# Optimization experiments

Hardware: AMD Instinct MI355X
Metric: run time of the kernel (lower is better)

The kernel has to match this reference:

```python
import jax, jax.numpy as jnp
import numpy as np

H = 768       # hidden_size
NH = 12       # num query heads
NKV = 4       # num kv heads
HD = 64       # head_dim
EPS = 1e-12

def setup_inputs() -> dict:
    key = jax.random.key(0)
    ks = jax.random.split(key, 6)
    s = 0.02
    return {
        "hidden_states": jax.random.normal(ks[0], (2, 2048, H), dtype=jnp.float32),
        "Wq": jax.random.normal(ks[1], (H, H), dtype=jnp.float32) * s,
        "bq": jnp.zeros((H,), jnp.float32),
        "Wk": jax.random.normal(ks[2], (H, NKV * HD), dtype=jnp.float32) * s,
        "bk": jnp.zeros((NKV * HD,), jnp.float32),
        "Wv": jax.random.normal(ks[3], (H, NKV * HD), dtype=jnp.float32) * s,
        "bv": jnp.zeros((NKV * HD,), jnp.float32),
        "Wo": jax.random.normal(ks[4], (H, H), dtype=jnp.float32) * s,
        "bo": jnp.zeros((H,), jnp.float32),
        "gamma": jnp.ones((H,), jnp.float32),
        "beta": jnpp if False else jnp.zeros((H,), jnp.float32),
    }

def _rope_tables(seq_len):
    # freqs over half the head dim, base 10000 (matches _init_rope)
    freqs = 1.0 / (10000.0 ** (jnp.arange(0, HD, 2, dtype=jnp.float32) / HD))  # [HD/2]
    t = jnp.arange(seq_len, dtype=jnp.float32)
    ang = jnp.outer(t, freqs)  # [S, HD/2]
    return jnp.cos(ang), jnp.sin(ang)

def _apply_rope(x, cos, sin):
    # x: [B, S, nheads, HD]; cos/sin: [S, HD/2] broadcast to [1, S, 1, HD/2]
    c = cos[None, :, None, :]
    s = sin[None, :, None, :]
    x1, x2 = x[..., : HD // 2], x[..., HD // 2 :]
    return jnp.concatenate([x1 * c - x2 * s, x1 * s + x2 * c], axis=-1)

def reference(hidden_states, Wq, bq, Wk, bk, Wv, bv, Wo, bo, gamma, beta):
    B, S, _ = hidden_states.shape
    residual = hidden_states
    # LayerNorm (eps=1e-12)
    mu = jnp.mean(hidden_states, axis=-1, keepdims=True)
    var = jnp.mean((hidden_states - mu) ** 2, axis=-1, keepdims=True)
    h = (hidden_states - mu) / jnp.sqrt(var + EPS) * gamma + beta
    q = (h @ Wq + bq).reshape(B, S, NH, HD)
    k = (h @ Wk + bk).reshape(B, S, NKV, HD)
    v = (h @ Wv + bv).reshape(B, S, NKV, HD)
    cos, sin = _rope_tables(S)
    q = _apply_rope(q, cos, sin)
    k = _apply_rope(k, cos, sin)
    # GQA: repeat_interleave kv heads to match query heads
    rep = NH // NKV
    k = jnp.repeat(k, rep, axis=2)  # [B,S,NH,HD]
    v = jnp.repeat(v, rep, axis=2)
    # [B,NH,S,S] scores
    scores = jnp.einsum("bqhd,bkhd->bhqk", q, k) / jnp.sqrt(jnp.float32(HD))
    attn = jax.nn.softmax(scores, axis=-1)
    out = jnp.einsum("bhqk,bkhd->bqhd", attn, v).reshape(B, S, H)
    out = out @ Wo + bo
    return residual + out
```

## Files before the change

kernel.cpp:

```cpp
#include <hip/hip_runtime.h>

typedef short bf16x8 __attribute__((ext_vector_type(8)));
typedef float f32x4 __attribute__((ext_vector_type(4)));
typedef float f32x16 __attribute__((ext_vector_type(16)));
typedef unsigned u32x4 __attribute__((ext_vector_type(4)));

#define SWZ(r, cb) ((((int)(r)) << 7) + (((int)(cb)) ^ ((((int)(r)) & 7) << 4)))

__device__ __forceinline__ unsigned short f2b(float f) {
    unsigned u = __builtin_bit_cast(unsigned, f);
    u = (u + 0x7FFFu + ((u >> 16) & 1u)) >> 16;
    return (unsigned short)u;
}
__device__ __forceinline__ float b2f(unsigned short h) {
    unsigned u = ((unsigned)h) << 16;
    return __builtin_bit_cast(float, u);
}
__device__ __forceinline__ void gload16(void* lds, const void* gsrc) {
    __builtin_amdgcn_global_load_lds((const __attribute__((address_space(1))) void*)gsrc,
                                     (__attribute__((address_space(3))) void*)lds, 16, 0, 0);
}

__global__ __launch_bounds__(256) void ln_kernel(const float* __restrict__ x,
                                                 const float* __restrict__ gamma,
// ... 60 lines not shown
        tile[kr][nc + 0] = f.x; tile[kr][nc + 1] = f.y;
        tile[kr][nc + 2] = f.z; tile[kr][nc + 3] = f.w;
    }
    __syncthreads();
#pragma unroll
    for (int i = 0; i < 2; i++) {
        int nr = (t >> 3) + i * 32, kc = (t & 7) * 8;
        bf16x8 o;
#pragma unroll
        for (int j = 0; j < 8; j++) o[j] = (short)f2b(tile[kc + j][nr]);
        *(bf16x8*)(WT + (size_t)(n0 + nr) * 768 + k0 + kc) = o;
    }
}

__global__ __launch_bounds__(256) void gemm_qkv(const unsigned short* __restrict__ A,
                                                const unsigned short* __restrict__ WqT,
                                                const unsigned short* __restrict__ WkT,
                                                const unsigned short* __restrict__ WvT,
                                                const float* __restrict__ bq,
                                                const float* __restrict__ bk,
                                                const float* __restrict__ bv,
                                                unsigned short* __restrict__ qo,
                                                unsigned short* __restrict__ kfrag,
                                                unsigned short* __restrict__ vfrag) {
    __shared__ __align__(1024) char smem[65536];
    const int m0 = blockIdx.x * 128;
    const int n0 = blockIdx.y * 128;
    const unsigned short* WT; const float* bias; int c0;
    if (n0 < 768)       { WT = WqT + (size_t)n0 * 768;          bias = bq; c0 = n0;        }
    else if (n0 < 1024) { WT = WkT + (size_t)(n0 - 768) * 768;  bias = bk; c0 = n0 - 768;  }
    else                { WT = WvT + (size_t)(n0 - 1024) * 768; bias = bv; c0 = n0 - 1024; }
    const int tid = threadIdx.x, lane = tid & 63, w = tid >> 6;
    const int wr = w >> 1, wc = w & 1;
    const int l15 = lane & 15;
    const int rl = lane >> 3, cl = lane & 7;
    const int scol = (cl * 16) ^ (rl << 4);

    const char* srcA0 = (const char*)A  + (size_t)(m0 + w * 32 +  0 + rl) * 1536 + scol;
    const char* srcA1 = (const char*)A  + (size_t)(m0 + w * 32 +  8 + rl) * 1536 + scol;
    const char* srcA2 = (const char*)A  + (size_t)(m0 + w * 32 + 16 + rl) * 1536 + scol;
    const char* srcA3 = (const char*)A  + (size_t)(m0 + w * 32 + 24 + rl) * 1536 + scol;
    const char* srcB0 = (const char*)WT + (size_t)(w * 32 +  0 + rl) * 1536 + scol;
    const char* srcB1 = (const char*)WT + (size_t)(w * 32 +  8 + rl) * 1536 + scol;
    const char* srcB2 = (const char*)WT + (size_t)(w * 32 + 16 + rl) * 1536 + scol;
    const char* srcB3 = (const char*)WT + (size_t)(w * 32 + 24 + rl) * 1536 + scol;
    const int cb = w * 4096;

    f32x4 acc[4][4];
#pragma unroll
    for (int m = 0; m < 4; m++)
#pragma unroll
        for (int n = 0; n < 4; n++) acc[m][n] = (f32x4){0.f, 0.f, 0.f, 0.f};

    gload16(smem + cb +    0, srcA0); gload16(smem + cb + 1024, srcA1);
    gload16(smem + cb + 2048, srcA2); gload16(smem + cb + 3072, srcA3);
    gload16(smem + 32768 + cb +    0, srcB0); gload16(smem + 32768 + cb + 1024, srcB1);
    gload16(smem + 32768 + cb + 2048, srcB2); gload16(smem + 32768 + cb + 3072, srcB3);
    __syncthreads();

    for (int t = 0; t < 12; ++t) {
        const int cur = t & 1;
        if (t < 11) {
            srcA0 += 128; srcA1 += 128; srcA2 += 128; srcA3 += 128;
            srcB0 += 128; srcB1 += 128; srcB2 += 128; srcB3 += 128;
            char* ab = smem + (cur ^ 1) * 16384 + cb;
            char* bb = smem + 32768 + (cur ^ 1) * 16384 + cb;
            gload16(ab +    0, srcA0); gload16(ab + 1024, srcA1);
            gload16(ab + 2048, srcA2); gload16(ab + 3072, srcA3);
            gload16(bb +    0, srcB0); gload16(bb + 1024, srcB1);
            gload16(bb + 2048, srcB2); gload16(bb + 3072, srcB3);
        }
        const char* Ab = smem + cur * 16384;
        const char* Bb = smem + 32768 + cur * 16384;
#pragma unroll
        for (int ks = 0; ks < 2; ks++) {
            bf16x8 a[4], b[4];
#pragma unroll
            for (int m = 0; m < 4; m++)
                a[m] = *(const bf16x8*)(Ab + SWZ(wr * 64 + m * 16 + l15, (lane >> 4) * 16 + ks * 64));
#pragma unroll
            for (int n = 0; n < 4; n++)
                b[n] = *(const bf16x8*)(Bb + SWZ(wc * 64 + n * 16 + l15, (lane >> 4) * 16 + ks * 64));
#pragma unroll
            for (int m = 0; m < 4; m++)
#pragma unroll
                for (int n = 0; n < 4; n++)
                    acc[m][n] = __builtin_amdgcn_mfma_f32_16x16x32_bf16(a[m], b[n], acc[m][n], 0, 0, 0);
        }
        __syncthreads();
    }

    if (n0 >= 1024) {
#pragma unroll
        for (int n = 0; n < 4; n++) {
            int col = c0 + wc * 64 + n * 16 + l15;
            float bs = bias[col];
            int g = col >> 6, d = col & 63;
            int hd = d >> 5, ld = d & 31;
#pragma unroll
            for (int m = 0; m < 4; m++) {
                int row = m0 + wr * 64 + m * 16 + ((lane >> 4) << 2);
                int bb2 = row >> 11, srow = row & 2047;
                int tt = srow >> 6, kvc = srow & 63;
                int s = kvc >> 4, hl = (kvc >> 3) & 1, j0 = kvc & 7;
                ushort4 o;
                o.x = f2b(acc[m][n][0] + bs); o.y = f2b(acc[m][n][1] + bs);
                o.z = f2b(acc[m][n][2] + bs); o.w = f2b(acc[m][n][3] + bs);
                *(ushort4*)((char*)vfrag + ((size_t)((bb2 * 4 + g) * 32 + tt)) * 8192 +
                            (2 * s + hd) * 1024 + (hl * 32 + ld) * 16 + j0 * 2) = o;
            }
        }
    } else if (n0 >= 768) {
#pragma unroll
        for (int n = 0; n < 2; n++) {
            int col = c0 + wc * 64 + n * 16 + l15;
            float bs1 = bias[col], bs2 = bias[col + 32];
            int g = col >> 6, i = col & 63;
            float freq = exp2f(-(float)i * (13.287712379549449f / 32.0f));
            int s = i >> 4, h2k = (i >> 3) & 1, j = i & 7;
            int laneoff = (h2k * 32 + 0) * 16 + j * 2;
#pragma unroll
            for (int m = 0; m < 4; m++) {
#pragma unroll
                for (int r = 0; r < 4; r++) {
                    int row = m0 + wr * 64 + m * 16 + ((lane >> 4) << 2) + r;
                    int bb2 = row >> 11, srow = row & 2047;
                    int tt = srow >> 6, kvr = srow & 63, hk = kvr >> 5, lkv = kvr & 31;
                    float sn, cs;
                    sincosf((float)srow * freq, &sn, &cs);
                    float x1 = acc[m][n][r] + bs1, x2 = acc[m][n + 2][r] + bs2;
                    size_t base = ((size_t)((bb2 * 4 + g) * 32 + tt)) * 8192 + laneoff + lkv * 16;
                    *(unsigned short*)((char*)kfrag + base + (2 * s + hk) * 1024)     = f2b(x1 * cs - x2 * sn);
                    *(unsigned short*)((char*)kfrag + base + (2 * s + 4 + hk) * 1024) = f2b(x1 * sn + x2 * cs);
                }
            }
        }
    } else {
#pragma unroll
        for (int n = 0; n < 4; n++) {
            int col = c0 + wc * 64 + n * 16 + l15;
            float bs = bias[col];
#pragma unroll
            for (int m = 0; m < 4; m++) {
#pragma unroll
                for (int r = 0; r < 4; r++) {
                    int row = m0 + wr * 64 + m * 16 + ((lane >> 4) << 2) + r;
                    qo[(size_t)row * 768 + col] = f2b(acc[m][n][r] + bs);
                }
            }
        }
    }
}

__global__ __launch_bounds__(768) void flashkv_kernel(const unsigned short* __restrict__ qb,
                                                      const unsigned short* __restrict__ kfrag,
                                                      const unsigned short* __restrict__ vfrag,
                                                      unsigned short* __restrict__ ob) {
    __shared__ __align__(1024) char smem[65536];
    const int s0 = blockIdx.x * 64;
    const int bg = blockIdx.y, b = bg >> 2;
    const int tid = threadIdx.x, lane = tid & 63, w = tid >> 6;
    const int h2 = lane >> 5, l31 = lane & 31;
    const int hq = w >> 2, qsub = (w >> 1) & 1, half = w & 1;
    const int hh = (bg & 3) * 3 + hq;

    const char* kf = (const char*)kfrag + (size_t)bg * 262144;
    const char* vf = (const char*)vfrag + (size_t)bg * 262144;
    const int ncha = (w < 8) ? 3 : 2;
    const char* srcs[3]; int ldss[3];
#pragma unroll
    for (int i = 0; i < 3; i++) {
        int c = w + i * 12;
        if (c < 32) {
            int hf = c >> 4, cc = c & 15;
            const char* basep = (cc < 8) ? kf : vf;
            srcs[i] = basep + (size_t)(hf * 16) * 8192 + (cc & 7) * 1024 + lane * 16;
            ldss[i] = hf * 32768 + ((cc < 8) ? 0 : 16384) + (cc & 7) * 1024;
        } else { srcs[i] = kf; ldss[i] = 0; }
    }

#pragma unroll
    for (int i = 0; i < 3; i++)
        if (i < ncha) gload16(smem + ldss[i], srcs[i]);

    const int qrow = s0 + qsub * 32 + l31;
    const unsigned short* qbase = qb + ((size_t)(b * 2048 + qrow) * 12 + hh) * 64 + 8 * h2;
    bf16x8 qr[4];
#pragma unroll
    for (int s = 0; s < 4; s++) qr[s] = *(const bf16x8*)(qbase + 16 * s);
    bf16x8 bqf[4];
    {
        const float SC = 0.125f * 1.4426950408889634f;
#pragma unroll
        for (int s = 0; s < 2; s++)
#pragma unroll
            for (int j = 0; j < 8; j++) {
                int i = 16 * s + 8 * h2 + j;
                float freq = exp2f(-(float)i * (13.287712379549449f / 32.0f));
                float sn, cs;
                sincosf((float)qrow * freq, &sn, &cs);
                float x1 = b2f((unsigned short)qr[s][j]);
                float x2 = b2f((unsigned short)qr[s + 2][j]);
                bqf[s][j]     = (short)f2b((x1 * cs - x2 * sn) * SC);
                bqf[s + 2][j] = (short)f2b((x1 * sn + x2 * cs) * SC);
            }
    }

    f32x16 accO0, accO1, cinit;
#pragma unroll
    for (int r = 0; r < 16; r++) { accO0[r] = 0.f; accO1[r] = 0.f; cinit[r] = -24.0f; }
    float l_r = 0.f;

    __syncthreads();

    for (int t = 0; t < 16; ++t) {
        const int cur = t & 1;
        if (t < 15) {
            const int nb = (cur ^ 1) * 8192;
#pragma unroll
            for (int i = 0; i < 3; i++)
                if (i < ncha) { srcs[i] += 8192; gload16(smem + ldss[i] + nb, srcs[i]); }
        }
        const char* kb_ = smem + half * 32768 + cur * 8192 + lane * 16;
        const char* vb_ = smem + half * 32768 + 16384 + cur * 8192 + lane * 16;

        f32x16 sc0, sc1;
        __builtin_amdgcn_s_setprio(1);
        sc0 = __builtin_amdgcn_mfma_f32_32x32x16_bf16(*(const bf16x8*)(kb_ + 0),    bqf[0], cinit, 0, 0, 0);
        sc1 = __builtin_amdgcn_mfma_f32_32x32x16_bf16(*(const bf16x8*)(kb_ + 1024), bqf[0], cinit, 0, 0, 0);
#pragma unroll
        for (int s = 1; s < 4; s++) {
            sc0 = __builtin_amdgcn_mfma_f32_32x32x16_bf16(*(const bf16x8*)(kb_ + s * 2048),        bqf[s], sc0, 0, 0, 0);
            sc1 = __builtin_amdgcn_mfma_f32_32x32x16_bf16(*(const bf16x8*)(kb_ + s * 2048 + 1024), bqf[s], sc1, 0, 0, 0);
        }
        __builtin_amdgcn_s_setprio(0);

#pragma unroll
        for (int r = 0; r < 16; r++) { sc0[r] = __builtin_amdgcn_exp2f(sc0[r]); }
#pragma unroll
        for (int r = 0; r < 16; r++) { sc1[r] = __builtin_amdgcn_exp2f(sc1[r]); }
        float ps[8];
#pragma unroll
        for (int r = 0; r < 8; r++)
            ps[r] = (sc0[r] + sc0[r + 8]) + (sc1[r] + sc1[r + 8]);
        float ls = ((ps[0] + ps[1]) + (ps[2] + ps[3])) + ((ps[4] + ps[5]) + (ps[6] + ps[7]));
        ls += __shfl_xor(ls, 32, 64);
        l_r += ls;

        __builtin_amdgcn_s_setprio(1);
#define DO_FRAG(SCX, OFF, S)                                                                  \
        {                                                                                     \
            unsigned A0, A1, B0, B1;                                                          \
            asm("v_cvt_pk_bf16_f32 %0, %1, %2" : "=v"(A0) : "v"(SCX[OFF + 0]), "v"(SCX[OFF + 1])); \
            asm("v_cvt_pk_bf16_f32 %0, %1, %2" : "=v"(A1) : "v"(SCX[OFF + 2]), "v"(SCX[OFF + 3])); \
            asm("v_cvt_pk_bf16_f32 %0, %1, %2" : "=v"(B0) : "v"(SCX[OFF + 4]), "v"(SCX[OFF + 5])); \
            asm("v_cvt_pk_bf16_f32 %0, %1, %2" : "=v"(B1) : "v"(SCX[OFF + 6]), "v"(SCX[OFF + 7])); \
            asm volatile("v_permlane32_swap_b32 %0, %1" : "+v"(A0), "+v"(B0));                 \
            asm volatile("v_permlane32_swap_b32 %0, %1" : "+v"(A1), "+v"(B1));                 \
            u32x4 fd = {A0, A1, B0, B1};                                                      \
            bf16x8 pa = __builtin_bit_cast(bf16x8, fd);                                       \
            bf16x8 bv0 = *(const bf16x8*)(vb_ + (S) * 2048);                                  \
            bf16x8 bv1 = *(const bf16x8*)(vb_ + (S) * 2048 + 1024);                           \
            accO0 = __builtin_amdgcn_mfma_f32_32x32x16_bf16(pa, bv0, accO0, 0, 0, 0);         \
            accO1 = __builtin_amdgcn_mfma_f32_32x32x16_bf16(pa, bv1, accO1, 0, 0, 0);         \
        }
        DO_FRAG(sc0, 0, 0)
        DO_FRAG(sc0, 8, 1)
        DO_FRAG(sc1, 0, 2)
        DO_FRAG(sc1, 8, 3)
#undef DO_FRAG
        __builtin_amdgcn_s_setprio(0);
        __syncthreads();
    }

    const int pr = w >> 1;
    if (half) {
        if (h2 == 0) *(float*)(smem + 49152 + pr * 128 + l31 * 4) = l_r;
#pragma unroll
        for (int pc = 0; pc < 4; pc++) {
            float4 f0;
            f0.x = accO0[4 * pc]; f0.y = accO0[4 * pc + 1];
            f0.z = accO0[4 * pc + 2]; f0.w = accO0[4 * pc + 3];
            *(float4*)(smem + pr * 8192 + pc * 1024 + lane * 16) = f0;
            float4 f1;
            f1.x = accO1[4 * pc]; f1.y = accO1[4 * pc + 1];
            f1.z = accO1[4 * pc + 2]; f1.w = accO1[4 * pc + 3];
            *(float4*)(smem + pr * 8192 + (4 + pc) * 1024 + lane * 16) = f1;
        }
    }
    __syncthreads();
    if (!half) {
        float lt = l_r + *(const float*)(smem + 49152 + pr * 128 + l31 * 4);
        f32x16 po0, po1;
#pragma unroll
        for (int pc = 0; pc < 4; pc++) {
            float4 f0 = *(const float4*)(smem + pr * 8192 + pc * 1024 + lane * 16);
            po0[4 * pc] = f0.x; po0[4 * pc + 1] = f0.y; po0[4 * pc + 2] = f0.z; po0[4 * pc + 3] = f0.w;
            float4 f1 = *(const float4*)(smem + pr * 8192 + (4 + pc) * 1024 + lane * 16);
            po1[4 * pc] = f1.x; po1[4 * pc + 1] = f1.y; po1[4 * pc + 2] = f1.z; po1[4 * pc + 3] = f1.w;
        }
#pragma unroll
        for (int r = 0; r < 16; r++) {
            int qc = (r & 3) + 8 * (r >> 2) + 4 * h2;
            float lvr = __builtin_amdgcn_rcpf(__shfl(lt, qc, 64));
            int row = s0 + qsub * 32 + qc;
            size_t basei = ((size_t)(b * 2048 + row) * 12 + hh) * 64;
            ob[basei + l31]      = f2b((accO0[r] + po0[r]) * lvr);
            ob[basei + 32 + l31] = f2b((accO1[r] + po1[r]) * lvr);
        }
    }
}

__global__ __launch_bounds__(256) void gemm_out(const unsigned short* __restrict__ A,
                                                const unsigned short* __restrict__ WoT,
                                                const float* __restrict__ bo,
                                                const float* __restrict__ resid,
                                                float* __restrict__ out) {
    __shared__ __align__(1024) char smem[65536];
    const int m0 = blockIdx.x * 128;
    const int n0 = blockIdx.y * 128;
    const int tid = threadIdx.x, lane = tid & 63, w = tid >> 6;
    const int wr = w >> 1, wc = w & 1;
    const int rl = lane >> 3, cl = lane & 7;
    const int scol = (cl * 16) ^ (rl << 4);

    const char* srcA0 = (const char*)A + (size_t)(m0 + w * 32 +  0 + rl) * 1536 + scol;
    const char* srcA1 = (const char*)A + (size_t)(m0 + w * 32 +  8 + rl) * 1536 + scol;
    const char* srcA2 = (const char*)A + (size_t)(m0 + w * 32 + 16 + rl) * 1536 + scol;
    const char* srcA3 = (const char*)A + (size_t)(m0 + w * 32 + 24 + rl) * 1536 + scol;
    const char* srcB0 = (const char*)WoT + (size_t)(n0 + w * 32 +  0 + rl) * 1536 + scol;
    const char* srcB1 = (const char*)WoT + (size_t)(n0 + w * 32 +  8 + rl) * 1536 + scol;
    const char* srcB2 = (const char*)WoT + (size_t)(n0 + w * 32 + 16 + rl) * 1536 + scol;
    const char* srcB3 = (const char*)WoT + (size_t)(n0 + w * 32 + 24 + rl) * 1536 + scol;
    const int cb = w * 4096;

    f32x4 acc[4][4];
#pragma unroll
    for (int m = 0; m < 4; m++)
#pragma unroll
        for (int n = 0; n < 4; n++) acc[m][n] = (f32x4){0.f, 0.f, 0.f, 0.f};

    gload16(smem + cb +    0, srcA0); gload16(smem + cb + 1024, srcA1);
    gload16(smem + cb + 2048, srcA2); gload16(smem + cb + 3072, srcA3);
    gload16(smem + 32768 + cb +    0, srcB0); gload16(smem + 32768 + cb + 1024, srcB1);
    gload16(smem + 32768 + cb + 2048, srcB2); gload16(smem + 32768 + cb + 3072, srcB3);
    __syncthreads();

    for (int t = 0; t < 12; ++t) {
        const int cur = t & 1;
        if (t < 11) {
            srcA0 += 128; srcA1 += 128; srcA2 += 128; srcA3 += 128;
            srcB0 += 128; srcB1 += 128; srcB2 += 128; srcB3 += 128;
            char* ab = smem + (cur ^ 1) * 16384 + cb;
            char* bb = smem + 32768 + (cur ^ 1) * 16384 + cb;
            gload16(ab +    0, srcA0); gload16(ab + 1024, srcA1);
            gload16(ab + 2048, srcA2); gload16(ab + 3072, srcA3);
            gload16(bb +    0, srcB0); gload16(bb + 1024, srcB1);
            gload16(bb + 2048, srcB2); gload16(bb + 3072, srcB3);
        }
        const char* Ab = smem + cur * 16384;
        const char* Bb = smem + 32768 + cur * 16384;
#pragma unroll
        for (int ks = 0; ks < 2; ks++) {
            bf16x8 a[4], b[4];
#pragma unroll
            for (int m = 0; m < 4; m++)
                a[m] = *(const bf16x8*)(Ab + SWZ(wr * 64 + m * 16 + (lane & 15), (lane >> 4) * 16 + ks * 64));
#pragma unroll
            for (int n = 0; n < 4; n++)
                b[n] = *(const bf16x8*)(Bb + SWZ(wc * 64 + n * 16 + (lane & 15), (lane >> 4) * 16 + ks * 64));
#pragma unroll
            for (int m = 0; m < 4; m++)
#pragma unroll
                for (int n = 0; n < 4; n++)
                    acc[m][n] = __builtin_amdgcn_mfma_f32_16x16x32_bf16(a[m], b[n], acc[m][n], 0, 0, 0);
        }
        __syncthreads();
    }
#pragma unroll
    for (int n = 0; n < 4; n++) {
        int col = n0 + wc * 64 + n * 16 + (lane & 15);
        float bs = bo[col];
#pragma unroll
        for (int m = 0; m < 4; m++) {
#pragma unroll
            for (int r = 0; r < 4; r++) {
                int row = m0 + wr * 64 + m * 16 + ((lane >> 4) << 2) + r;
                out[(size_t)row * 768 + col] = acc[m][n][r] + bs + resid[(size_t)row * 768 + col];
            }
        }
    }
}

extern "C" void kernel_launch(void* const* d_in, const int* in_sizes, int n_in,
                              void* d_out, int out_size, void* d_ws, size_t ws_size,
                              hipStream_t stream) {
    const float* hs    = (const float*)d_in[0];
    const float* Wq    = (const float*)d_in[1];
    const float* bq    = (const float*)d_in[2];
    const float* Wk    = (const float*)d_in[3];
    const float* bk    = (const float*)d_in[4];
    const float* Wv    = (const float*)d_in[5];
    const float* bv    = (const float*)d_in[6];
    const float* Wo    = (const float*)d_in[7];
    const float* bo    = (const float*)d_in[8];
    const float* gamma = (const float*)d_in[9];
    const float* beta  = (const float*)d_in[10];
    float* out = (float*)d_out;

    char* p = (char*)d_ws;
    unsigned short* hbuf  = (unsigned short*)p; p += (size_t)4096 * 768 * 2;
    unsigned short* qbuf  = (unsigned short*)p; p += (size_t)4096 * 768 * 2;
    unsigned short* kfbuf = (unsigned short*)p; p += (size_t)4096 * 256 * 2;
    unsigned short* vfbuf = (unsigned short*)p; p += (size_t)4096 * 256 * 2;
    unsigned short* WqT = (unsigned short*)p; p += (size_t)768 * 768 * 2;
    unsigned short* WkT = (unsigned short*)p; p += (size_t)256 * 768 * 2;
    unsigned short* WvT = (unsigned short*)p; p += (size_t)256 * 768 * 2;
    unsigned short* WoT = (unsigned short*)p; p += (size_t)768 * 768 * 2;
    unsigned short* obuf = hbuf;

    ln_kernel<<<1024, 256, 0, stream>>>(hs, gamma, beta, hbuf);
    transw_kernel<<<dim3(12, 12, 4), 256, 0, stream>>>(Wq, Wk, Wv, Wo, WqT, WkT, WvT, WoT);
    gemm_qkv<<<dim3(32, 10), 256, 0, stream>>>(hbuf, WqT, WkT, WvT, bq, bk, bv, qbuf, kfbuf, vfbuf);
    flashkv_kernel<<<dim3(32, 8), 768, 0, stream>>>(qbuf, kfbuf, vfbuf, obuf);
    gemm_out<<<dim3(32, 6), 256, 0, stream>>>(obuf, WoT, bo, hs, out);
}
```

Measured before the change: 86.60 us.

## Process all three GQA query heads per wave to reuse each K/V fragment

The attention kernel drops from 768 threads (12 waves, one query head per wave) to 256 threads (4 waves), each wave handling all three query heads that share a KV head. Each K and V fragment read from LDS now feeds three MFMAs instead of one, which cuts LDS read traffic and reuses the RoPE sin/cos values across heads. The cost is far more registers per wave (six output accumulators plus three score tiles), fewer waves to hide latency, and each wave issuing eight async copies per tile instead of two or three.

Measured after the change: 94.06 us. 8.6% more time.

```diff
diff --git a/kernel.cpp b/kernel.cpp
--- a/kernel.cpp
+++ b/kernel.cpp
@@ -236,161 +236,217 @@
     }
 }
 
-__global__ __launch_bounds__(768) void flashkv_kernel(const unsigned short* __restrict__ qb,
-                                                      const unsigned short* __restrict__ kfrag,
-                                                      const unsigned short* __restrict__ vfrag,
-                                                      unsigned short* __restrict__ ob) {
+__global__ __launch_bounds__(256, 1) void flash4_kernel(const unsigned short* __restrict__ qb,
+                                                        const unsigned short* __restrict__ kfrag,
+                                                        const unsigned short* __restrict__ vfrag,
+                                                        unsigned short* __restrict__ ob) {
     __shared__ __align__(1024) char smem[65536];
     const int s0 = blockIdx.x * 64;
     const int bg = blockIdx.y, b = bg >> 2;
     const int tid = threadIdx.x, lane = tid & 63, w = tid >> 6;
     const int h2 = lane >> 5, l31 = lane & 31;
-    const int hq = w >> 2, qsub = (w >> 1) & 1, half = w & 1;
-    const int hh = (bg & 3) * 3 + hq;
+    const int qsub = w >> 1, half = w & 1;
+    const int hbase = (bg & 3) * 3;
 
     const char* kf = (const char*)kfrag + (size_t)bg * 262144;
     const char* vf = (const char*)vfrag + (size_t)bg * 262144;
-    const int ncha = (w < 8) ? 3 : 2;
-    const char* srcs[3]; int ldss[3];
-#pragma unroll
-    for (int i = 0; i < 3; i++) {
-        int c = w + i * 12;
-        if (c < 32) {
-            int hf = c >> 4, cc = c & 15;
-            const char* basep = (cc < 8) ? kf : vf;
-            srcs[i] = basep + (size_t)(hf * 16) * 8192 + (cc & 7) * 1024 + lane * 16;
-            ldss[i] = hf * 32768 + ((cc < 8) ? 0 : 16384) + (cc & 7) * 1024;
-        } else { srcs[i] = kf; ldss[i] = 0; }
-    }
-
-#pragma unroll
-    for (int i = 0; i < 3; i++)
-        if (i < ncha) gload16(smem + ldss[i], srcs[i]);
+    const char* srcs[8]; int ldss[8];
+#pragma unroll
+    for (int i = 0; i < 8; i++) {
+        int c = w + i * 4;
+        int hf = c >> 4, cc = c & 15;
+        const char* basep = (cc < 8) ? kf : vf;
+        srcs[i] = basep + (size_t)(hf * 16) * 8192 + (cc & 7) * 1024 + lane * 16;
+        ldss[i] = hf * 32768 + ((cc < 8) ? 0 : 16384) + (cc & 7) * 1024;
+    }
+#pragma unroll
+    for (int i = 0; i < 8; i++) gload16(smem + ldss[i], srcs[i]);
 
     const int qrow = s0 + qsub * 32 + l31;
-    const unsigned short* qbase = qb + ((size_t)(b * 2048 + qrow) * 12 + hh) * 64 + 8 * h2;
-    bf16x8 qr[4];
-#pragma unroll
-    for (int s = 0; s < 4; s++) qr[s] = *(const bf16x8*)(qbase + 16 * s);
-    bf16x8 bqf[4];
+    bf16x8 qf[3][4];
     {
         const float SC = 0.125f * 1.4426950408889634f;
+        float cs_[16], sn_[16];
 #pragma unroll
         for (int s = 0; s < 2; s++)
 #pragma unroll
             for (int j = 0; j < 8; j++) {
                 int i = 16 * s + 8 * h2 + j;
                 float freq = exp2f(-(float)i * (13.287712379549449f / 32.0f));
-                float sn, cs;
-                sincosf((float)qrow * freq, &sn, &cs);
-                float x1 = b2f((unsigned short)qr[s][j]);
-                float x2 = b2f((unsigned short)qr[s + 2][j]);
-                bqf[s][j]     = (short)f2b((x1 * cs - x2 * sn) * SC);
-                bqf[s + 2][j] = (short)f2b((x1 * sn + x2 * cs) * SC);
-            }
-    }
-
-    f32x16 accO0, accO1, cinit;
-#pragma unroll
-    for (int r = 0; r < 16; r++) { accO0[r] = 0.f; accO1[r] = 0.f; cinit[r] = -24.0f; }
-    float l_r = 0.f;
+                sincosf((float)qrow * freq, &sn_[s * 8 + j], &cs_[s * 8 + j]);
+            }
+#pragma unroll
+        for (int u = 0; u < 3; u++) {
+            const unsigned short* qbase = qb + ((size_t)(b * 2048 + qrow) * 12 + hbase + u) * 64 + 8 * h2;
+            bf16x8 q0 = *(const bf16x8*)(qbase);
+            bf16x8 q1 = *(const bf16x8*)(qbase + 16);
+            bf16x8 q2 = *(const bf16x8*)(qbase + 32);
+            bf16x8 q3 = *(const bf16x8*)(qbase + 48);
+#pragma unroll
+            for (int j = 0; j < 8; j++) {
+                float x1 = b2f((unsigned short)q0[j]), x2 = b2f((unsigned short)q2[j]);
+                qf[u][0][j] = (short)f2b((x1 * cs_[j] - x2 * sn_[j]) * SC);
+                qf[u][2][j] = (short)f2b((x1 * sn_[j] + x2 * cs_[j]) * SC);
+                float y1 = b2f((unsigned short)q1[j]), y2 = b2f((unsigned short)q3[j]);
+                qf[u][1][j] = (short)f2b((y1 * cs_[8 + j] - y2 * sn_[8 + j]) * SC);
+                qf[u][3][j] = (short)f2b((y1 * sn_[8 + j] + y2 * cs_[8 + j]) * SC);
+            }
+        }
+    }
+
+    f32x16 acc[3][2], cinit;
+#pragma unroll
+    for (int u = 0; u < 3; u++)
+#pragma unroll
+        for (int k = 0; k < 2; k++)
+#pragma unroll
+            for (int r = 0; r < 16; r++) acc[u][k][r] = 0.f;
+#pragma unroll
+    for (int r = 0; r < 16; r++) cinit[r] = -24.0f;
+    float lr0 = 0.f, lr1 = 0.f, lr2 = 0.f;
 
     __syncthreads();
+
+#define SUM16(V) (((((V)[0]+(V)[1])+((V)[2]+(V)[3]))+(((V)[4]+(V)[5])+((V)[6]+(V)[7]))) + \
+                  ((((V)[8]+(V)[9])+((V)[10]+(V)[11]))+(((V)[12]+(V)[13])+((V)[14]+(V)[15]))))
 
     for (int t = 0; t < 16; ++t) {
         const int cur = t & 1;
         if (t < 15) {
             const int nb = (cur ^ 1) * 8192;
 #pragma unroll
-            for (int i = 0; i < 3; i++)
-                if (i < ncha) { srcs[i] += 8192; gload16(smem + ldss[i] + nb, srcs[i]); }
+            for (int i = 0; i < 8; i++) { srcs[i] += 8192; gload16(smem + ldss[i] + nb, srcs[i]); }
         }
         const char* kb_ = smem + half * 32768 + cur * 8192 + lane * 16;
-        const char* vb_ = smem + half * 32768 + 16384 + cur * 8192 + lane * 16;
-
-        f32x16 sc0, sc1;
-        __builtin_amdgcn_s_setprio(1);
-        sc0 = __builtin_amdgcn_mfma_f32_32x32x16_bf16(*(const bf16x8*)(kb_ + 0),    bqf[0], cinit, 0, 0, 0);
-        sc1 = __builtin_amdgcn_mfma_f32_32x32x16_bf16(*(const bf16x8*)(kb_ + 1024), bqf[0], cinit, 0, 0, 0);
-#pragma unroll
-        for (int s = 1; s < 4; s++) {
-            sc0 = __builtin_amdgcn_mfma_f32_32x32x16_bf16(*(const bf16x8*)(kb_ + s * 2048),        bqf[s], sc0, 0, 0, 0);
-            sc1 = __builtin_amdgcn_mfma_f32_32x32x16_bf16(*(const bf16x8*)(kb_ + s * 2048 + 1024), bqf[s], sc1, 0, 0, 0);
-        }
-        __builtin_amdgcn_s_setprio(0);
-
-#pragma unroll
-        for (int r = 0; r < 16; r++) { sc0[r] = __builtin_amdgcn_exp2f(sc0[r]); }
-#pragma unroll
-        for (int r = 0; r < 16; r++) { sc1[r] = __builtin_amdgcn_exp2f(sc1[r]); }
-        float ps[8];
-#pragma unroll
-        for (int r = 0; r < 8; r++)
-            ps[r] = (sc0[r] + sc0[r + 8]) + (sc1[r] + sc1[r + 8]);
-        float ls = ((ps[0] + ps[1]) + (ps[2] + ps[3])) + ((ps[4] + ps[5]) + (ps[6] + ps[7]));
-        ls += __shfl_xor(ls, 32, 64);
-        l_r += ls;
-
-        __builtin_amdgcn_s_setprio(1);
-#define DO_FRAG(SCX, OFF, S)                                                                  \
-        {                                                                                     \
-            unsigned A0, A1, B0, B1;                                                          \
-            asm("v_cvt_pk_bf16_f32 %0, %1, %2" : "=v"(A0) : "v"(SCX[OFF + 0]), "v"(SCX[OFF + 1])); \
-            asm("v_cvt_pk_bf16_f32 %0, %1, %2" : "=v"(A1) : "v"(SCX[OFF + 2]), "v"(SCX[OFF + 3])); \
-            asm("v_cvt_pk_bf16_f32 %0, %1, %2" : "=v"(B0) : "v"(SCX[OFF + 4]), "v"(SCX[OFF + 5])); \
-            asm("v_cvt_pk_bf16_f32 %0, %1, %2" : "=v"(B1) : "v"(SCX[OFF + 6]), "v"(SCX[OFF + 7])); \
-            asm volatile("v_permlane32_swap_b32 %0, %1" : "+v"(A0), "+v"(B0));                 \
-            asm volatile("v_permlane32_swap_b32 %0, %1" : "+v"(A1), "+v"(B1));                 \
-            u32x4 fd = {A0, A1, B0, B1};                                                      \
-            bf16x8 pa = __builtin_bit_cast(bf16x8, fd);                                       \
-            bf16x8 bv0 = *(const bf16x8*)(vb_ + (S) * 2048);                                  \
-            bf16x8 bv1 = *(const bf16x8*)(vb_ + (S) * 2048 + 1024);                           \
-            accO0 = __builtin_amdgcn_mfma_f32_32x32x16_bf16(pa, bv0, accO0, 0, 0, 0);         \
-            accO1 = __builtin_amdgcn_mfma_f32_32x32x16_bf16(pa, bv1, accO1, 0, 0, 0);         \
-        }
-        DO_FRAG(sc0, 0, 0)
-        DO_FRAG(sc0, 8, 1)
-        DO_FRAG(sc1, 0, 2)
-        DO_FRAG(sc1, 8, 3)
-#undef DO_FRAG
-        __builtin_amdgcn_s_setprio(0);
+        const char* vb_ = kb_ + 16384;
+
+#pragma unroll
+        for (int kvb = 0; kvb < 2; kvb++) {
+            f32x16 s0c, s1c, s2c;
+            __builtin_amdgcn_s_setprio(1);
+            {
+                bf16x8 ak = *(const bf16x8*)(kb_ + kvb * 1024);
+                s0c = __builtin_amdgcn_mfma_f32_32x32x16_bf16(ak, qf[0][0], cinit, 0, 0, 0);
+                s1c = __builtin_amdgcn_mfma_f32_32x32x16_bf16(ak, qf[1][0], cinit, 0, 0, 0);
+                s2c = __builtin_amdgcn_mfma_f32_32x32x16_bf16(ak, qf[2][0], cinit, 0, 0, 0);
+            }
+#pragma unroll
+            for (int s = 1; s < 4; s++) {
+                bf16x8 ak = *(const bf16x8*)(kb_ + s * 2048 + kvb * 1024);
+                s0c = __builtin_amdgcn_mfma_f32_32x32x16_bf16(ak, qf[0][s], s0c, 0, 0, 0);
+                s1c = __builtin_amdgcn_mfma_f32_32x32x16_bf16(ak, qf[1][s], s1c, 0, 0, 0);
+                s2c = __builtin_amdgcn_mfma_f32_32x32x16_bf16(ak, qf[2][s], s2c, 0, 0, 0);
+            }
+            __builtin_amdgcn_s_setprio(0);
+
+#pragma unroll
+            for (int r = 0; r < 16; r++) s0c[r] = __builtin_amdgcn_exp2f(s0c[r]);
+#pragma unroll
+            for (int r = 0; r < 16; r++) s1c[r] = __builtin_amdgcn_exp2f(s1c[r]);
+#pragma unroll
+            for (int r = 0; r < 16; r++) s2c[r] = __builtin_amdgcn_exp2f(s2c[r]);
+            lr0 += SUM16(s0c); lr1 += SUM16(s1c); lr2 += SUM16(s2c);
+
+            __builtin_amdgcn_s_setprio(1);
+#pragma unroll
+            for (int sh = 0; sh < 2; sh++) {
+                const int off = sh * 8;
+                bf16x8 pa0, pa1, pa2;
+                {
+                    unsigned A0, A1, B0, B1;
+                    asm("v_cvt_pk_bf16_f32 %0, %1, %2" : "=v"(A0) : "v"(s0c[off + 0]), "v"(s0c[off + 1]));
+                    asm("v_cvt_pk_bf16_f32 %0, %1, %2" : "=v"(A1) : "v"(s0c[off + 2]), "v"(s0c[off + 3]));
+                    asm("v_cvt_pk_bf16_f32 %0, %1, %2" : "=v"(B0) : "v"(s0c[off + 4]), "v"(s0c[off + 5]));
+                    asm("v_cvt_pk_bf16_f32 %0, %1, %2" : "=v"(B1) : "v"(s0c[off + 6]), "v"(s0c[off + 7]));
+                    asm volatile("v_permlane32_swap_b32 %0, %1" : "+v"(A0), "+v"(B0));
+                    asm volatile("v_permlane32_swap_b32 %0, %1" : "+v"(A1), "+v"(B1));
+                    u32x4 fd = {A0, A1, B0, B1};
+                    pa0 = __builtin_bit_cast(bf16x8, fd);
+                }
+                {
+                    unsigned A0, A1, B0, B1;
+                    asm("v_cvt_pk_bf16_f32 %0, %1, %2" : "=v"(A0) : "v"(s1c[off + 0]), "v"(s1c[off + 1]));
+                    asm("v_cvt_pk_bf16_f32 %0, %1, %2" : "=v"(A1) : "v"(s1c[off + 2]), "v"(s1c[off + 3]));
+                    asm("v_cvt_pk_bf16_f32 %0, %1, %2" : "=v"(B0) : "v"(s1c[off + 4]), "v"(s1c[off + 5]));
+                    asm("v_cvt_pk_bf16_f32 %0, %1, %2" : "=v"(B1) : "v"(s1c[off + 6]), "v"(s1c[off + 7]));
+                    asm volatile("v_permlane32_swap_b32 %0, %1" : "+v"(A0), "+v"(B0));
+                    asm volatile("v_permlane32_swap_b32 %0, %1" : "+v"(A1), "+v"(B1));
+                    u32x4 fd = {A0, A1, B0, B1};
+                    pa1 = __builtin_bit_cast(bf16x8, fd);
+                }
+                {
+                    unsigned A0, A1, B0, B1;
+                    asm("v_cvt_pk_bf16_f32 %0, %1, %2" : "=v"(A0) : "v"(s2c[off + 0]), "v"(s2c[off + 1]));
+                    asm("v_cvt_pk_bf16_f32 %0, %1, %2" : "=v"(A1) : "v"(s2c[off + 2]), "v"(s2c[off + 3]));
+                    asm("v_cvt_pk_bf16_f32 %0, %1, %2" : "=v"(B0) : "v"(s2c[off + 4]), "v"(s2c[off + 5]));
+                    asm("v_cvt_pk_bf16_f32 %0, %1, %2" : "=v"(B1) : "v"(s2c[off + 6]), "v"(s2c[off + 7]));
+                    asm volatile("v_permlane32_swap_b32 %0, %1" : "+v"(A0), "+v"(B0));
+                    asm volatile("v_permlane32_swap_b32 %0, %1" : "+v"(A1), "+v"(B1));
+                    u32x4 fd = {A0, A1, B0, B1};
+                    pa2 = __builtin_bit_cast(bf16x8, fd);
+                }
+                bf16x8 bv0 = *(const bf16x8*)(vb_ + (kvb * 2 + sh) * 2048);
+                bf16x8 bv1 = *(const bf16x8*)(vb_ + (kvb * 2 + sh) * 2048 + 1024);
+                acc[0][0] = __builtin_amdgcn_mfma_f32_32x32x16_bf16(pa0, bv0, acc[0][0], 0, 0, 0);
+                acc[0][1] = __builtin_amdgcn_mfma_f32_32x32x16_bf16(pa0, bv1, acc[0][1], 0, 0, 0);
+                acc[1][0] = __builtin_amdgcn_mfma_f32_32x32x16_bf16(pa1, bv0, acc[1][0], 0, 0, 0);
+                acc[1][1] = __builtin_amdgcn_mfma_f32_32x32x16_bf16(pa1, bv1, acc[1][1], 0, 0, 0);
+                acc[2][0] = __builtin_amdgcn_mfma_f32_32x32x16_bf16(pa2, bv0, acc[2][0], 0, 0, 0);
+                acc[2][1] = __builtin_amdgcn_mfma_f32_32x32x16_bf16(pa2, bv1, acc[2][1], 0, 0, 0);
+            }
+            __builtin_amdgcn_s_setprio(0);
+        }
         __syncthreads();
     }
-
-    const int pr = w >> 1;
+#undef SUM16
+
+    lr0 += __shfl_xor(lr0, 32, 64);
+    lr1 += __shfl_xor(lr1, 32, 64);
+    lr2 += __shfl_xor(lr2, 32, 64);
+
     if (half) {
-        if (h2 == 0) *(float*)(smem + 49152 + pr * 128 + l31 * 4) = l_r;
-#pragma unroll
-        for (int pc = 0; pc < 4; pc++) {
-            float4 f0;
-            f0.x = accO0[4 * pc]; f0.y = accO0[4 * pc + 1];
-            f0.z = accO0[4 * pc + 2]; f0.w = accO0[4 * pc + 3];
-            *(float4*)(smem + pr * 8192 + pc * 1024 + lane * 16) = f0;
-            float4 f1;
-            f1.x = accO1[4 * pc]; f1.y = accO1[4 * pc + 1];
-            f1.z = accO1[4 * pc + 2]; f1.w = accO1[4 * pc + 3];
-            *(float4*)(smem + pr * 8192 + (4 + pc) * 1024 + lane * 16) = f1;
-        }
+        if (h2 == 0) {
+            *(float*)(smem + 49152 + (qsub * 3 + 0) * 128 + l31 * 4) = lr0;
+            *(float*)(smem + 49152 + (qsub * 3 + 1) * 128 + l31 * 4) = lr1;
+            *(float*)(smem + 49152 + (qsub * 3 + 2) * 128 + l31 * 4) = lr2;
+        }
+#pragma unroll
+        for (int u = 0; u < 3; u++)
+#pragma unroll
+            for (int k = 0; k < 2; k++)
+#pragma unroll
+                for (int pc = 0; pc < 4; pc++) {
+                    float4 f;
+                    f.x = acc[u][k][4 * pc + 0]; f.y = acc[u][k][4 * pc + 1];
+                    f.z = acc[u][k][4 * pc + 2]; f.w = acc[u][k][4 * pc + 3];
+                    *(float4*)(smem + qsub * 24576 + (u * 2 + k) * 4096 + pc * 1024 + lane * 16) = f;
+                }
     }
     __syncthreads();
     if (!half) {
-        float lt = l_r + *(const float*)(smem + 49152 + pr * 128 + l31 * 4);
-        f32x16 po0, po1;
-#pragma unroll
-        for (int pc = 0; pc < 4; pc++) {
-            float4 f0 = *(const float4*)(smem + pr * 8192 + pc * 1024 + lane * 16);
-            po0[4 * pc] = f0.x; po0[4 * pc + 1] = f0.y; po0[4 * pc + 2] = f0.z; po0[4 * pc + 3] = f0.w;
-            float4 f1 = *(const float4*)(smem + pr * 8192 + (4 + pc) * 1024 + lane * 16);
-            po1[4 * pc] = f1.x; po1[4 * pc + 1] = f1.y; po1[4 * pc + 2] = f1.z; po1[4 * pc + 3] = f1.w;
-        }
-#pragma unroll
-        for (int r = 0; r < 16; r++) {
-            int qc = (r & 3) + 8 * (r >> 2) + 4 * h2;
-            float lvr = __builtin_amdgcn_rcpf(__shfl(lt, qc, 64));
-            int row = s0 + qsub * 32 + qc;
-            size_t basei = ((size_t)(b * 2048 + row) * 12 + hh) * 64;
-            ob[basei + l31]      = f2b((accO0[r] + po0[r]) * lvr);
-            ob[basei + 32 + l31] = f2b((accO1[r] + po1[r]) * lvr);
+        float lt0 = lr0 + *(const float*)(smem + 49152 + (qsub * 3 + 0) * 128 + l31 * 4);
+        float lt1 = lr1 + *(const float*)(smem + 49152 + (qsub * 3 + 1) * 128 + l31 * 4);
+        float lt2 = lr2 + *(const float*)(smem + 49152 + (qsub * 3 + 2) * 128 + l31 * 4);
+#pragma unroll
+        for (int u = 0; u < 3; u++) {
+            f32x16 po0, po1;
+#pragma unroll
+            for (int pc = 0; pc < 4; pc++) {
+                float4 f0 = *(const float4*)(smem + qsub * 24576 + (u * 2 + 0) * 4096 + pc * 1024 + lane * 16);
+                po0[4 * pc + 0] = f0.x; po0[4 * pc + 1] = f0.y; po0[4 * pc + 2] = f0.z; po0[4 * pc + 3] = f0.w;
+                float4 f1 = *(const float4*)(smem + qsub * 24576 + (u * 2 + 1) * 4096 + pc * 1024 + lane * 16);
+                po1[4 * pc + 0] = f1.x; po1[4 * pc + 1] = f1.y; po1[4 * pc + 2] = f1.z; po1[4 * pc + 3] = f1.w;
+            }
+            float ltu = (u == 0) ? lt0 : ((u == 1) ? lt1 : lt2);
+#pragma unroll
+            for (int r = 0; r < 16; r++) {
+                int qc = (r & 3) + 8 * (r >> 2) + 4 * h2;
+                float lv = __builtin_amdgcn_rcpf(__shfl(ltu, qc, 64));
+                int row = s0 + qsub * 32 + qc;
+                size_t basei = ((size_t)(b * 2048 + row) * 12 + hbase + u) * 64;
+                ob[basei + l31]      = f2b((acc[u][0][r] + po0[r]) * lv);
+                ob[basei + 32 + l31] = f2b((acc[u][1][r] + po1[r]) * lv);
+            }
         }
     }
 }
@@ -506,6 +562,6 @@
     ln_kernel<<<1024, 256, 0, stream>>>(hs, gamma, beta, hbuf);
     transw_kernel<<<dim3(12, 12, 4), 256, 0, stream>>>(Wq, Wk, Wv, Wo, WqT, WkT, WvT, WoT);
     gemm_qkv<<<dim3(32, 10), 256, 0, stream>>>(hbuf, WqT, WkT, WvT, bq, bk, bv, qbuf, kfbuf, vfbuf);
-    flashkv_kernel<<<dim3(32, 8), 768, 0, stream>>>(qbuf, kfbuf, vfbuf, obuf);
+    flash4_kernel<<<dim3(32, 8), 256, 0, stream>>>(qbuf, kfbuf, vfbuf, obuf);
     gemm_out<<<dim3(32, 6), 256, 0, stream>>>(obuf, WoT, bo, hs, out);
 }
```

## Split attention KV range across four waves per head with 32-row query tiles

Applied to the files above, without the earlier changes.

The attention kernel now gives each block 32 query rows instead of 64, doubling the grid from 256 to 512 blocks. Each wave handles one head over a quarter of the key sequence, where before two waves split it in halves. The partial outputs and row sums are combined in a two-stage shared-memory reduction. The goal is better CU occupancy (512 blocks on a 256-CU part) and fewer scores per wave per iteration, at the cost of reloading K/V for twice as many blocks and extra reduction syncs.

After: 132.0 us. +52.4%, slower.

```diff
diff --git a/kernel.cpp b/kernel.cpp
--- a/kernel.cpp
+++ b/kernel.cpp
@@ -236,161 +236,185 @@
     }
 }
 
-__global__ __launch_bounds__(768) void flashkv_kernel(const unsigned short* __restrict__ qb,
-                                                      const unsigned short* __restrict__ kfrag,
-                                                      const unsigned short* __restrict__ vfrag,
-                                                      unsigned short* __restrict__ ob) {
+__global__ __launch_bounds__(768, 6) void flashq_kernel(const unsigned short* __restrict__ qb,
+                                                        const unsigned short* __restrict__ kfrag,
+                                                        const unsigned short* __restrict__ vfrag,
+                                                        unsigned short* __restrict__ ob) {
     __shared__ __align__(1024) char smem[65536];
-    const int s0 = blockIdx.x * 64;
+    const int s0 = blockIdx.x * 32;
     const int bg = blockIdx.y, b = bg >> 2;
     const int tid = threadIdx.x, lane = tid & 63, w = tid >> 6;
     const int h2 = lane >> 5, l31 = lane & 31;
-    const int hq = w >> 2, qsub = (w >> 1) & 1, half = w & 1;
+    const int hq = w >> 2, qt = w & 3;
     const int hh = (bg & 3) * 3 + hq;
 
-    const char* kf = (const char*)kfrag + (size_t)bg * 262144;
-    const char* vf = (const char*)vfrag + (size_t)bg * 262144;
-    const int ncha = (w < 8) ? 3 : 2;
-    const char* srcs[3]; int ldss[3];
-#pragma unroll
-    for (int i = 0; i < 3; i++) {
-        int c = w + i * 12;
-        if (c < 32) {
-            int hf = c >> 4, cc = c & 15;
-            const char* basep = (cc < 8) ? kf : vf;
-            srcs[i] = basep + (size_t)(hf * 16) * 8192 + (cc & 7) * 1024 + lane * 16;
-            ldss[i] = hf * 32768 + ((cc < 8) ? 0 : 16384) + (cc & 7) * 1024;
-        } else { srcs[i] = kf; ldss[i] = 0; }
-    }
-
-#pragma unroll
-    for (int i = 0; i < 3; i++)
-        if (i < ncha) gload16(smem + ldss[i], srcs[i]);
-
-    const int qrow = s0 + qsub * 32 + l31;
-    const unsigned short* qbase = qb + ((size_t)(b * 2048 + qrow) * 12 + hh) * 64 + 8 * h2;
-    bf16x8 qr[4];
-#pragma unroll
-    for (int s = 0; s < 4; s++) qr[s] = *(const bf16x8*)(qbase + 16 * s);
-    bf16x8 bqf[4];
+    const bool stager = (w < 8);
+    const int sj = w >> 1, isV = w & 1;
+    const char* gsrc0 = (isV ? (const char*)vfrag : (const char*)kfrag) + (size_t)bg * 262144 + lane * 16;
+    const long gstr  = isV ? 1024 : 2048;
+    const int  goff1 = isV ? 4096 : 1024;
+    const int  lds_st = sj * 16384 + (isV ? 4096 : 0);
+
+    if (stager) {
+        int T = sj * 16;
+        const char* gb = gsrc0 + (size_t)(T >> 1) * 8192 + (T & 1) * goff1;
+#pragma unroll
+        for (int i = 0; i < 4; i++) gload16(smem + lds_st + i * 1024, gb + i * gstr);
+    }
+
+    const int qrow = s0 + l31;
+    bf16x8 qf[4];
     {
         const float SC = 0.125f * 1.4426950408889634f;
-#pragma unroll
-        for (int s = 0; s < 2; s++)
-#pragma unroll
-            for (int j = 0; j < 8; j++) {
-                int i = 16 * s + 8 * h2 + j;
-                float freq = exp2f(-(float)i * (13.287712379549449f / 32.0f));
-                float sn, cs;
-                sincosf((float)qrow * freq, &sn, &cs);
-                float x1 = b2f((unsigned short)qr[s][j]);
-                float x2 = b2f((unsigned short)qr[s + 2][j]);
-                bqf[s][j]     = (short)f2b((x1 * cs - x2 * sn) * SC);
-                bqf[s + 2][j] = (short)f2b((x1 * sn + x2 * cs) * SC);
-            }
-    }
-
-    f32x16 accO0, accO1, cinit;
-#pragma unroll
-    for (int r = 0; r < 16; r++) { accO0[r] = 0.f; accO1[r] = 0.f; cinit[r] = -24.0f; }
-    float l_r = 0.f;
-
-    __syncthreads();
+        const unsigned short* qbase = qb + ((size_t)(b * 2048 + qrow) * 12 + hh) * 64 + 8 * h2;
+        bf16x8 q0 = *(const bf16x8*)(qbase);
+        bf16x8 q1 = *(const bf16x8*)(qbase + 16);
+        bf16x8 q2 = *(const bf16x8*)(qbase + 32);
+        bf16x8 q3 = *(const bf16x8*)(qbase + 48);
+#pragma unroll
+        for (int j = 0; j < 8; j++) {
+            int i0 = 8 * h2 + j;
+            float f0 = exp2f(-(float)i0 * (13.287712379549449f / 32.0f));
+            float sn0, cs0;
+            sincosf((float)qrow * f0, &sn0, &cs0);
+            float x1 = b2f((unsigned short)q0[j]), x2 = b2f((unsigned short)q2[j]);
+            qf[0][j] = (short)f2b((x1 * cs0 - x2 * sn0) * SC);
+            qf[2][j] = (short)f2b((x1 * sn0 + x2 * cs0) * SC);
+            int i1 = 16 + 8 * h2 + j;
+            float f1 = exp2f(-(float)i1 * (13.287712379549449f / 32.0f));
+            float sn1, cs1;
+            sincosf((float)qrow * f1, &sn1, &cs1);
+            float y1 = b2f((unsigned short)q1[j]), y2 = b2f((unsigned short)q3[j]);
+            qf[1][j] = (short)f2b((y1 * cs1 - y2 * sn1) * SC);
+            qf[3][j] = (short)f2b((y1 * sn1 + y2 * cs1) * SC);
+        }
+    }
+
+    f32x16 acc0, acc1, cinit;
+#pragma unroll
+    for (int r = 0; r < 16; r++) { acc0[r] = 0.f; acc1[r] = 0.f; cinit[r] = -24.0f; }
+    float lr = 0.f;
+
+    __syncthreads();
+
+#define SUM16(V) (((((V)[0]+(V)[1])+((V)[2]+(V)[3]))+(((V)[4]+(V)[5])+((V)[6]+(V)[7]))) + \
+                  ((((V)[8]+(V)[9])+((V)[10]+(V)[11]))+(((V)[12]+(V)[13])+((V)[14]+(V)[15]))))
 
     for (int t = 0; t < 16; ++t) {
         const int cur = t & 1;
-        if (t < 15) {
-            const int nb = (cur ^ 1) * 8192;
-#pragma unroll
-            for (int i = 0; i < 3; i++)
-                if (i < ncha) { srcs[i] += 8192; gload16(smem + ldss[i] + nb, srcs[i]); }
-        }
-        const char* kb_ = smem + half * 32768 + cur * 8192 + lane * 16;
-        const char* vb_ = smem + half * 32768 + 16384 + cur * 8192 + lane * 16;
-
-        f32x16 sc0, sc1;
+        if (t < 15 && stager) {
+            int T = sj * 16 + t + 1;
+            const char* gb = gsrc0 + (size_t)(T >> 1) * 8192 + (T & 1) * goff1;
+            char* ld = smem + lds_st + (cur ^ 1) * 8192;
+#pragma unroll
+            for (int i = 0; i < 4; i++) gload16(ld + i * 1024, gb + i * gstr);
+        }
+        const char* kb_ = smem + qt * 16384 + cur * 8192 + lane * 16;
+        const char* vb_ = kb_ + 4096;
+
+        f32x16 sc;
         __builtin_amdgcn_s_setprio(1);
-        sc0 = __builtin_amdgcn_mfma_f32_32x32x16_bf16(*(const bf16x8*)(kb_ + 0),    bqf[0], cinit, 0, 0, 0);
-        sc1 = __builtin_amdgcn_mfma_f32_32x32x16_bf16(*(const bf16x8*)(kb_ + 1024), bqf[0], cinit, 0, 0, 0);
-#pragma unroll
-        for (int s = 1; s < 4; s++) {
-            sc0 = __builtin_amdgcn_mfma_f32_32x32x16_bf16(*(const bf16x8*)(kb_ + s * 2048),        bqf[s], sc0, 0, 0, 0);
-            sc1 = __builtin_amdgcn_mfma_f32_32x32x16_bf16(*(const bf16x8*)(kb_ + s * 2048 + 1024), bqf[s], sc1, 0, 0, 0);
-        }
+        sc = __builtin_amdgcn_mfma_f32_32x32x16_bf16(*(const bf16x8*)(kb_), qf[0], cinit, 0, 0, 0);
+#pragma unroll
+        for (int s = 1; s < 4; s++)
+            sc = __builtin_amdgcn_mfma_f32_32x32x16_bf16(*(const bf16x8*)(kb_ + s * 1024), qf[s], sc, 0, 0, 0);
         __builtin_amdgcn_s_setprio(0);
 
 #pragma unroll
-        for (int r = 0; r < 16; r++) { sc0[r] = __builtin_amdgcn_exp2f(sc0[r]); }
-#pragma unroll
-        for (int r = 0; r < 16; r++) { sc1[r] = __builtin_amdgcn_exp2f(sc1[r]); }
-        float ps[8];
-#pragma unroll
-        for (int r = 0; r < 8; r++)
-            ps[r] = (sc0[r] + sc0[r + 8]) + (sc1[r] + sc1[r + 8]);
-        float ls = ((ps[0] + ps[1]) + (ps[2] + ps[3])) + ((ps[4] + ps[5]) + (ps[6] + ps[7]));
-        ls += __shfl_xor(ls, 32, 64);
-        l_r += ls;
+        for (int r = 0; r < 16; r++) sc[r] = __builtin_amdgcn_exp2f(sc[r]);
+        lr += SUM16(sc);
 
         __builtin_amdgcn_s_setprio(1);
-#define DO_FRAG(SCX, OFF, S)                                                                  \
-        {                                                                                     \
-            unsigned A0, A1, B0, B1;                                                          \
-            asm("v_cvt_pk_bf16_f32 %0, %1, %2" : "=v"(A0) : "v"(SCX[OFF + 0]), "v"(SCX[OFF + 1])); \
-            asm("v_cvt_pk_bf16_f32 %0, %1, %2" : "=v"(A1) : "v"(SCX[OFF + 2]), "v"(SCX[OFF + 3])); \
-            asm("v_cvt_pk_bf16_f32 %0, %1, %2" : "=v"(B0) : "v"(SCX[OFF + 4]), "v"(SCX[OFF + 5])); \
-            asm("v_cvt_pk_bf16_f32 %0, %1, %2" : "=v"(B1) : "v"(SCX[OFF + 6]), "v"(SCX[OFF + 7])); \
-            asm volatile("v_permlane32_swap_b32 %0, %1" : "+v"(A0), "+v"(B0));                 \
-            asm volatile("v_permlane32_swap_b32 %0, %1" : "+v"(A1), "+v"(B1));                 \
-            u32x4 fd = {A0, A1, B0, B1};                                                      \
-            bf16x8 pa = __builtin_bit_cast(bf16x8, fd);                                       \
-            bf16x8 bv0 = *(const bf16x8*)(vb_ + (S) * 2048);                                  \
-            bf16x8 bv1 = *(const bf16x8*)(vb_ + (S) * 2048 + 1024);                           \
-            accO0 = __builtin_amdgcn_mfma_f32_32x32x16_bf16(pa, bv0, accO0, 0, 0, 0);         \
-            accO1 = __builtin_amdgcn_mfma_f32_32x32x16_bf16(pa, bv1, accO1, 0, 0, 0);         \
-        }
-        DO_FRAG(sc0, 0, 0)
-        DO_FRAG(sc0, 8, 1)
-        DO_FRAG(sc1, 0, 2)
-        DO_FRAG(sc1, 8, 3)
-#undef DO_FRAG
+#pragma unroll
+        for (int sh = 0; sh < 2; sh++) {
+            const int off = sh * 8;
+            unsigned A0, A1, B0, B1;
+            asm("v_cvt_pk_bf16_f32 %0, %1, %2" : "=v"(A0) : "v"(sc[off + 0]), "v"(sc[off + 1]));
+            asm("v_cvt_pk_bf16_f32 %0, %1, %2" : "=v"(A1) : "v"(sc[off + 2]), "v"(sc[off + 3]));
+            asm("v_cvt_pk_bf16_f32 %0, %1, %2" : "=v"(B0) : "v"(sc[off + 4]), "v"(sc[off + 5]));
+            asm("v_cvt_pk_bf16_f32 %0, %1, %2" : "=v"(B1) : "v"(sc[off + 6]), "v"(sc[off + 7]));
+            asm volatile("v_permlane32_swap_b32 %0, %1" : "+v"(A0), "+v"(B0));
+            asm volatile("v_permlane32_swap_b32 %0, %1" : "+v"(A1), "+v"(B1));
+            u32x4 fd = {A0, A1, B0, B1};
+            bf16x8 pa = __builtin_bit_cast(bf16x8, fd);
+            bf16x8 bv0 = *(const bf16x8*)(vb_ + (2 * sh + 0) * 1024);
+            bf16x8 bv1 = *(const bf16x8*)(vb_ + (2 * sh + 1) * 1024);
+            acc0 = __builtin_amdgcn_mfma_f32_32x32x16_bf16(pa, bv0, acc0, 0, 0, 0);
+            acc1 = __builtin_amdgcn_mfma_f32_32x32x16_bf16(pa, bv1, acc1, 0, 0, 0);
+        }
         __builtin_amdgcn_s_setprio(0);
         __syncthreads();
     }
-
-    const int pr = w >> 1;
-    if (half) {
-        if (h2 == 0) *(float*)(smem + 49152 + pr * 128 + l31 * 4) = l_r;
+#undef SUM16
+
+    lr += __shfl_xor(lr, 32, 64);
+
+    if (qt >= 2) {
+        int slot = hq * 2 + (qt - 2);
 #pragma unroll
         for (int pc = 0; pc < 4; pc++) {
             float4 f0;
-            f0.x = accO0[4 * pc]; f0.y = accO0[4 * pc + 1];
-            f0.z = accO0[4 * pc + 2]; f0.w = accO0[4 * pc + 3];
-            *(float4*)(smem + pr * 8192 + pc * 1024 + lane * 16) = f0;
+            f0.x = acc0[4 * pc + 0]; f0.y = acc0[4 * pc + 1];
+            f0.z = acc0[4 * pc + 2]; f0.w = acc0[4 * pc + 3];
+            *(float4*)(smem + slot * 8192 + pc * 1024 + lane * 16) = f0;
             float4 f1;
-            f1.x = accO1[4 * pc]; f1.y = accO1[4 * pc + 1];
-            f1.z = accO1[4 * pc + 2]; f1.w = accO1[4 * pc + 3];
-            *(float4*)(smem + pr * 8192 + (4 + pc) * 1024 + lane * 16) = f1;
-        }
-    }
-    __syncthreads();
-    if (!half) {
-        float lt = l_r + *(const float*)(smem + 49152 + pr * 128 + l31 * 4);
-        f32x16 po0, po1;
+            f1.x = acc1[4 * pc + 0]; f1.y = acc1[4 * pc + 1];
+            f1.z = acc1[4 * pc + 2]; f1.w = acc1[4 * pc + 3];
+            *(float4*)(smem + slot * 8192 + 4096 + pc * 1024 + lane * 16) = f1;
+        }
+        if (h2 == 0) *(float*)(smem + 49152 + slot * 128 + l31 * 4) = lr;
+    }
+    __syncthreads();
+    if (qt < 2) {
+        int slot = hq * 2 + qt;
 #pragma unroll
         for (int pc = 0; pc < 4; pc++) {
-            float4 f0 = *(const float4*)(smem + pr * 8192 + pc * 1024 + lane * 16);
-            po0[4 * pc] = f0.x; po0[4 * pc + 1] = f0.y; po0[4 * pc + 2] = f0.z; po0[4 * pc + 3] = f0.w;
-            float4 f1 = *(const float4*)(smem + pr * 8192 + (4 + pc) * 1024 + lane * 16);
-            po1[4 * pc] = f1.x; po1[4 * pc + 1] = f1.y; po1[4 * pc + 2] = f1.z; po1[4 * pc + 3] = f1.w;
-        }
+            float4 f0 = *(const float4*)(smem + slot * 8192 + pc * 1024 + lane * 16);
+            acc0[4 * pc + 0] += f0.x; acc0[4 * pc + 1] += f0.y;
+            acc0[4 * pc + 2] += f0.z; acc0[4 * pc + 3] += f0.w;
+            float4 f1 = *(const float4*)(smem + slot * 8192 + 4096 + pc * 1024 + lane * 16);
+            acc1[4 * pc + 0] += f1.x; acc1[4 * pc + 1] += f1.y;
+            acc1[4 * pc + 2] += f1.z; acc1[4 * pc + 3] += f1.w;
+        }
+        lr += *(const float*)(smem + 49152 + slot * 128 + l31 * 4);
+    }
+    __syncthreads();
+    if (qt == 1) {
+        int slot = hq;
+#pragma unroll
+        for (int pc = 0; pc < 4; pc++) {
+            float4 f0;
+            f0.x = acc0[4 * pc + 0]; f0.y = acc0[4 * pc + 1];
+            f0.z = acc0[4 * pc + 2]; f0.w = acc0[4 * pc + 3];
+            *(float4*)(smem + slot * 8192 + pc * 1024 + lane * 16) = f0;
+            float4 f1;
+            f1.x = acc1[4 * pc + 0]; f1.y = acc1[4 * pc + 1];
+            f1.z = acc1[4 * pc + 2]; f1.w = acc1[4 * pc + 3];
+            *(float4*)(smem + slot * 8192 + 4096 + pc * 1024 + lane * 16) = f1;
+        }
+        if (h2 == 0) *(float*)(smem + 50176 + slot * 128 + l31 * 4) = lr;
+    }
+    __syncthreads();
+    if (qt == 0) {
+        int slot = hq;
+#pragma unroll
+        for (int pc = 0; pc < 4; pc++) {
+            float4 f0 = *(const float4*)(smem + slot * 8192 + pc * 1024 + lane * 16);
+            acc0[4 * pc + 0] += f0.x; acc0[4 * pc + 1] += f0.y;
+            acc0[4 * pc + 2] += f0.z; acc0[4 * pc + 3] += f0.w;
+            float4 f1 = *(const float4*)(smem + slot * 8192 + 4096 + pc * 1024 + lane * 16);
+            acc1[4 * pc + 0] += f1.x; acc1[4 * pc + 1] += f1.y;
+            acc1[4 * pc + 2] += f1.z; acc1[4 * pc + 3] += f1.w;
+        }
+        lr += *(const float*)(smem + 50176 + slot * 128 + l31 * 4);
 #pragma unroll
         for (int r = 0; r < 16; r++) {
             int qc = (r & 3) + 8 * (r >> 2) + 4 * h2;
-            float lvr = __builtin_amdgcn_rcpf(__shfl(lt, qc, 64));
-            int row = s0 + qsub * 32 + qc;
+            float lv = __builtin_amdgcn_rcpf(__shfl(lr, qc, 64));
+            int row = s0 + qc;
             size_t basei = ((size_t)(b * 2048 + row) * 12 + hh) * 64;
-            ob[basei + l31]      = f2b((accO0[r] + po0[r]) * lvr);
-            ob[basei + 32 + l31] = f2b((accO1[r] + po1[r]) * lvr);
+            ob[basei + l31]      = f2b(acc0[r] * lv);
+            ob[basei + 32 + l31] = f2b(acc1[r] * lv);
         }
     }
 }
@@ -506,6 +530,6 @@
     ln_kernel<<<1024, 256, 0, stream>>>(hs, gamma, beta, hbuf);
     transw_kernel<<<dim3(12, 12, 4), 256, 0, stream>>>(Wq, Wk, Wv, Wo, WqT, WkT, WvT, WoT);
     gemm_qkv<<<dim3(32, 10), 256, 0, stream>>>(hbuf, WqT, WkT, WvT, bq, bk, bv, qbuf, kfbuf, vfbuf);
-    flashkv_kernel<<<dim3(32, 8), 768, 0, stream>>>(qbuf, kfbuf, vfbuf, obuf);
+    flashq_kernel<<<dim3(64, 8), 768, 0, stream>>>(qbuf, kfbuf, vfbuf, obuf);
     gemm_out<<<dim3(32, 6), 256, 0, stream>>>(obuf, WoT, bo, hs, out);
 }
```
